# Kernel optimization log

Measured on AMD Instinct MI355X. Metric: run time of the kernel, lower is better.

The kernel has to match this reference:

```python
import jax, jax.numpy as jnp
import numpy as np

DIM = 256
HEADS = 8
DIM_HEAD = 64
EPS = 1e-12  # F.normalize eps


def rms_norm(x, w, dim):
    # F.normalize over channel dim (axis=1) * weight * sqrt(dim)
    n = jnp.sqrt(jnp.sum(x * x, axis=1, keepdims=True))
    xn = x / jnp.maximum(n, EPS)
    return xn * w[None, :, None, None] * (dim ** 0.5)


def setup_inputs() -> dict:
    key = jax.random.key(0)
    ks = jax.random.split(key, 4)
    hd = HEADS * DIM_HEAD
    return {
        "x": jax.random.normal(ks[0], (16, DIM, 64, 64), dtype=jnp.float32),
        "norm_w": jnp.ones((DIM,), jnp.float32),
        "qkv_w": jax.random.normal(ks[1], (3 * hd, DIM), jnp.float32) * (DIM ** -0.5),
        "out_w": jax.random.normal(ks[2], (DIM, hd), jnp.float32) * (hd ** -0.5),
        "out_b": jnp.zeros((DIM,), jnp.float32),
        "out_norm_w": jnp.ones((DIM,), jnp.float32),
    }


def reference(x, norm_w, qkv_w, out_w, out_b, out_norm_w):
    b, c, H, W = x.shape
    n = H * W
    scale = DIM_HEAD ** -0.5

    xn = rms_norm(x, norm_w, DIM)
    # 1x1 conv == channel matmul: [3hd, c] x [b, c, H, W]
    qkv = jnp.einsum('oc,bchw->bohw', qkv_w, xn)
    q, k, v = jnp.split(qkv, 3, axis=1)

    def to_heads(t):
        # b (h d) x y -> b h d n
        return t.reshape(b, HEADS, DIM_HEAD, n)

    q = jax.nn.softmax(to_heads(q), axis=2) * scale  # softmax over feature dim d
    k = jax.nn.softmax(to_heads(k), axis=3)          # softmax over spatial n
    v = to_heads(v)

    ctx = jnp.einsum('bhdn,bhen->bhde', k, v)   # [b,h,d,e]
    out = jnp.einsum('bhde,bhdn->bhen', ctx, q) # [b,h,e,n]
    out = out.reshape(b, HEADS * DIM_HEAD, H, W)

    out = jnp.einsum('oc,bchw->bohw', out_w, out) + out_b[None, :, None, None]
    return rms_norm(out, out_norm_w, DIM)
```

## Files before the change

### kernel.cpp

```cpp
#include <hip/hip_runtime.h>

#define C_ 256
#define N_ 4096
#define NH_ 8

typedef unsigned short u16;
typedef unsigned int u32;
typedef __attribute__((ext_vector_type(8))) short s8v;
typedef __attribute__((ext_vector_type(4))) float f4v;

#define MFMA16 __builtin_amdgcn_mfma_f32_16x16x32_bf16

__device__ __forceinline__ float bf2f(u16 b){ union{u32 u; float f;} v; v.u=((u32)b)<<16; return v.f; }
__device__ __forceinline__ u16 f2bf(float f){ union{float f; u32 u;} v; v.f=f; return (u16)((v.u + 0x7FFFu + ((v.u>>16)&1u))>>16); }

__device__ __forceinline__ void gl_lds16(const u16* g, u16* l){
  __builtin_amdgcn_global_load_lds((const __attribute__((address_space(1))) u32*)g,
                                   (__attribute__((address_space(3))) u32*)l, 16, 0, 0);
}

__global__ __launch_bounds__(256) void k_prep(const float* __restrict__ x, const float* __restrict__ nw,
                                              u16* __restrict__ xnT){
  __shared__ float red[256];
  __shared__ float nws[256];
  const int tid = threadIdx.x;
  nws[tid] = nw[tid];
  const int blk = blockIdx.x, b = blk>>6, n0 = (blk&63)*64;
  const int cq = tid>>6, px = tid&63;
  const float* xp = x + (size_t)b*(C_*N_) + (size_t)(cq*64)*N_ + n0 + px;
  float v[64]; float s = 0.f;
  #pragma unroll
  for (int i=0;i<64;i++){ float t = xp[(size_t)i*N_]; v[i]=t; s = fmaf(t,t,s); }
  red[tid] = s;
  __syncthreads();
  const float st = red[px] + red[64+px] + red[128+px] + red[192+px];
  const float r = 16.0f / fmaxf(sqrtf(st), 1e-12f);
  u16* o = xnT + ((size_t)b*4096 + n0 + px)*256 + cq*64;
  #pragma unroll
  for (int i=0;i<64;i+=2){
    *(u32*)(o+i) = (u32)f2bf(v[i]*r*nws[cq*64+i]) | ((u32)f2bf(v[i+1]*r*nws[cq*64+i+1])<<16);
  }
}

__global__ __launch_bounds__(256) void k_wconv(const float* __restrict__ qkvw, const float* __restrict__ ow,
                                               u16* __restrict__ wqkv, u16* __restrict__ owb){
  int q = blockIdx.x*256 + threadIdx.x;
  int i = q*4;
  const float4 f4 = (i < 393216) ? *(const float4*)&qkvw[i] : *(const float4*)&ow[i-393216];
  u32 lo = (u32)f2bf(f4.x) | ((u32)f2bf(f4.y)<<16);
  u32 hi = (u32)f2bf(f4.z) | ((u32)f2bf(f4.w)<<16);
  u16* dst = (i < 393216) ? (wqkv + i) : (owb + (i-393216));
  *(u32*)dst = lo;
  *(u32*)(dst+2) = hi;
}

__global__ __launch_bounds__(256,3) void k_kv(const u16* __restrict__ xnT, const u16* __restrict__ wqkv,
    u16* __restrict__ ctxp, float* __restrict__ Mp, float* __restrict__ Sp){
  __shared__ u16 xs[64*256];
  __shared__ u16 pbuf[64*72];
  __shared__ u16 vbuf[64*72];
  const int idx = blockIdx.x;
  const int ch = idx&7, h = (idx>>3)&7, b = idx>>6;
  const int tid=threadIdx.x, w=tid>>6, l=tid&63, l15=l&15, lg=l>>4;
  const int swl = (l15&7)<<4;
  const u16* xb  = xnT + (size_t)b*(4096*256);
  const int srow = (l>>5);
  const int scolB = (l&31)*16;
  s8v ak[8], av[8];
  {
    const u16* wkp = wqkv + (size_t)(512 + h*64 + w*16 + l15)*256 + lg*8;
    #pragma unroll
    for (int cs=0; cs<8; cs++){ ak[cs] = *(const s8v*)(wkp + cs*32); av[cs] = *(const s8v*)(wkp + 131072 + cs*32); }
  }
  int colOff[8];
  #pragma unroll
  for (int cs=0; cs<8; cs++) colOff[cs] = (((cs<<6)+(lg<<4)) ^ swl)>>1;

  f4v acc[4];
  #pragma unroll
  for (int et=0;et<4;et++) acc[et] = (f4v){0.f,0.f,0.f,0.f};
  float ps[4] = {0.f,0.f,0.f,0.f};

  {
    const int n0 = ch*512;
    #pragma unroll
    for (int i=0;i<8;i++){
      int rloc = w*16 + i*2 + srow;
      int scol = scolB ^ ((rloc&7)<<4);
      gl_lds16(xb + (size_t)(n0+rloc)*256 + (scol>>1), &xs[(w*16+i*2)*256]);
    }
  }

  for (int t=0; t<8; ++t){
    __syncthreads();
    f4v kacc[4], vacc[4];
    #pragma unroll
    for (int ns=0;ns<4;ns++){ kacc[ns]=(f4v){0.f,0.f,0.f,0.f}; vacc[ns]=(f4v){0.f,0.f,0.f,0.f}; }
    #pragma unroll
    for (int cs=0; cs<8; cs++){
      #pragma unroll
      for (int ns=0; ns<4; ns++){
        s8v bfr = *(const s8v*)&xs[(ns*16+l15)*256 + colOff[cs]];
        kacc[ns] = MFMA16(ak[cs], bfr, kacc[ns], 0,0,0);
        vacc[ns] = MFMA16(av[cs], bfr, vacc[ns], 0,0,0);
      }
    }
    #pragma unroll
    for (int j=0;j<4;j++){
      const int row = w*16 + lg*4 + j;
      #pragma unroll
      for (int ns=0;ns<4;ns++){
        float e = __expf(kacc[ns][j] - 30.0f);
        ps[j] += e;
        pbuf[row*72 + ns*16+l15] = f2bf(e);
        vbuf[row*72 + ns*16+l15] = f2bf(vacc[ns][j]);
      }
    }
    __syncthreads();
    if (t<7){
      const int n0 = ch*512 + (t+1)*64;
      #pragma unroll
      for (int i=0;i<8;i++){
        int rloc = w*16 + i*2 + srow;
        int scol = scolB ^ ((rloc&7)<<4);
        gl_lds16(xb + (size_t)(n0+rloc)*256 + (scol>>1), &xs[(w*16+i*2)*256]);
      }
    }
    #pragma unroll
    for (int ks=0; ks<2; ks++){
      s8v af = *(const s8v*)(pbuf + (w*16+l15)*72 + ks*32 + lg*8);
      #pragma unroll
      for (int et=0; et<4; et++){
        s8v bv = *(const s8v*)(vbuf + (et*16+l15)*72 + ks*32 + lg*8);
        acc[et] = MFMA16(af, bv, acc[et], 0,0,0);
      }
    }
  }
  u16* cp = ctxp + (((size_t)ch*16 + b)*8 + h)*4096;
  #pragma unroll
  for (int et=0; et<4; et++)
    #pragma unroll
    for (int j=0;j<4;j++)
      cp[(w*16+lg*4+j)*64 + et*16+l15] = f2bf(acc[et][j]);
  #pragma unroll
  for (int j=0;j<4;j++){
    float s = ps[j];
    s += __shfl_xor(s,1); s += __shfl_xor(s,2);
    s += __shfl_xor(s,4); s += __shfl_xor(s,8);
    ps[j] = s;
  }
  if (l15==0){
    #pragma unroll
    for (int j=0;j<4;j++){
      int rg = (b*8+h)*64 + w*16 + lg*4 + j;
      Mp[ch*8192+rg]=30.0f; Sp[ch*8192+rg]=ps[j];
    }
  }
}

__global__ __launch_bounds__(256) void k_comb(const u16* __restrict__ ctxp, const float* __restrict__ Mp,
    const float* __restrict__ Sp, u16* __restrict__ ctxD){
  __shared__ float fs[8][64];
  __shared__ float iSs[64];
  const int bh = blockIdx.x, tid = threadIdx.x;
  if (tid < 64){
    float m[8];
    float Mg = -1e30f;
    #pragma unroll
    for (int ch=0;ch<8;ch++){ m[ch] = Mp[ch*8192 + bh*64 + tid]; Mg = fmaxf(Mg, m[ch]); }
    float Sg = 0.f;
    #pragma unroll
    for (int ch=0;ch<8;ch++){
      float fv = __expf(m[ch]-Mg);
      fs[ch][tid] = fv;
      Sg += Sp[ch*8192 + bh*64 + tid]*fv;
    }
    iSs[tid] = 1.0f / Sg;
  }
  __syncthreads();
  const int d = tid>>2, e0 = (tid&3)*16;
  u16* op = ctxD + (size_t)bh*4096 + d*64 + e0;
  const float fsc = iSs[d];
  #pragma unroll
  for (int i=0;i<16;i++){
    float v = 0.f;
    #pragma unroll
    for (int ch=0;ch<8;ch++)
      v += bf2f(ctxp[(size_t)ch*524288 + (size_t)bh*4096 + d*64 + e0+i]) * fs[ch][d];
    op[i] = f2bf(v * fsc);
  }
}

__global__ __launch_bounds__(256) void k_g(const u16* __restrict__ owb, const u16* __restrict__ ctxD,
                                           u16* __restrict__ G){
  const int bh = blockIdx.x, h = bh&7;
  const int tid = threadIdx.x, w = tid>>6, l = tid&63, l15 = l&15, lg = l>>4;
  s8v a[4][2], bD[4][2];
  #pragma unroll
  for (int mt=0; mt<4; mt++)
    #pragma unroll
    for (int ks=0; ks<2; ks++)
      a[mt][ks] = *(const s8v*)(owb + (size_t)(w*64+mt*16+l15)*512 + h*64 + ks*32 + lg*8);
  #pragma unroll
  for (int dt=0; dt<4; dt++)
    #pragma unroll
    for (int ks=0; ks<2; ks++)
      bD[dt][ks] = *(const s8v*)(ctxD + (size_t)bh*4096 + (dt*16+l15)*64 + ks*32 + lg*8);
  f4v acc[4][4];
  #pragma unroll
  for (int mt=0;mt<4;mt++)
    #pragma unroll
    for (int dt=0;dt<4;dt++) acc[mt][dt] = (f4v){0.f,0.f,0.f,0.f};
  #pragma unroll
  for (int ks=0; ks<2; ks++)
    #pragma unroll
    for (int mt=0; mt<4; mt++)
      #pragma unroll
      for (int dt=0; dt<4; dt++)
        acc[mt][dt] = MFMA16(a[mt][ks], bD[dt][ks], acc[mt][dt], 0,0,0);
  u16* gp = G + (size_t)bh*16384;
  #pragma unroll
  for (int mt=0; mt<4; mt++)
    #pragma unroll
    for (int dt=0; dt<4; dt++)
      #pragma unroll
      for (int j=0; j<4; j++)
        gp[(w*64 + mt*16 + lg*4 + j)*64 + dt*16 + l15] = f2bf(acc[mt][dt][j]);
}

__global__ __launch_bounds__(512,4) void k_qout(const u16* __restrict__ xnT, const u16* __restrict__ wqkv,
    const u16* __restrict__ Gg, const float* __restrict__ ob, const float* __restrict__ onw,
    float* __restrict__ out){
  __shared__ u16 WQ[64*256];
  __shared__ u16 Gs[256*64];
  __shared__ u16 qa[4][1024];
  __shared__ float pp[4][2][16];
  __shared__ float ssb[4][2][16];
  const int tid = threadIdx.x;
  const int w=tid>>6, l=tid&63, l15=l&15, lg=l>>4;
  const int g=w&3, half=w>>2;
  const int blk=blockIdx.x, b=blk>>6, n0=(blk&63)*64;
  const u16* xb = xnT + ((size_t)b*4096 + n0)*256;
  const u16* Gbase = Gg + (size_t)b*8*16384;
  u16* qag = qa[g];
  const int wqRow0 = (l>>5);
  const int wqColB = (l&31)*16;
  const int gRow0  = (l>>3);
  const int gColB  = (l&7)*16;
  s8v ax[8];
  #pragma unroll
  for (int cs=0;cs<8;cs++) ax[cs] = *(const s8v*)(xb + (size_t)(g*16+l15)*256 + cs*32 + lg*8);
  f4v oacc[8];
  #pragma unroll
  for (int mt=0;mt<8;mt++) oacc[mt] = (f4v){0.f,0.f,0.f,0.f};

  #pragma unroll
  for (int i=0;i<4;i++){
    int row = (i*8+w)*2 + wqRow0;
    int scol = wqColB ^ ((row&15)<<4);
    gl_lds16(wqkv + (size_t)row*256 + (scol>>1), &WQ[(i*8+w)*512]);
  }
  #pragma unroll
  for (int i=0;i<4;i++){
    int row = (i*8+w)*8 + gRow0;
    int scol = gColB ^ ((row&7)<<4);
    gl_lds16(Gbase + (size_t)row*64 + (scol>>1), &Gs[(i*8+w)*512]);
  }

  for (int h=0; h<8; ++h){
    __syncthreads();
    if (h>0){
      const u16* gg = Gbase + (size_t)h*16384;
      #pragma unroll
      for (int i=0;i<4;i++){
        int row = (i*8+w)*8 + gRow0;
        int scol = gColB ^ ((row&7)<<4);
        gl_lds16(gg + (size_t)row*64 + (scol>>1), &Gs[(i*8+w)*512]);
      }
    }
    f4v qacc[2];
    qacc[0] = (f4v){0.f,0.f,0.f,0.f};
    qacc[1] = (f4v){0.f,0.f,0.f,0.f};
    #pragma unroll
    for (int dt2=0; dt2<2; dt2++){
      const int drow = (half*2+dt2)*16 + l15;
      #pragma unroll
      for (int cs=0; cs<8; cs++){
        s8v bw = *(const s8v*)&WQ[drow*256 + ((((cs<<6)|(lg<<4)) ^ (l15<<4))>>1)];
        qacc[dt2] = MFMA16(ax[cs], bw, qacc[dt2], 0,0,0);
      }
    }
    float sj[4];
    #pragma unroll
    for (int j=0;j<4;j++){
      float e0 = __expf(qacc[0][j]-30.0f);
      float e1 = __expf(qacc[1][j]-30.0f);
      qacc[0][j]=e0; qacc[1][j]=e1;
      float s = e0+e1;
      s += __shfl_xor(s,1); s += __shfl_xor(s,2);
      s += __shfl_xor(s,4); s += __shfl_xor(s,8);
      sj[j] = s;
      if (l15==0) pp[g][half][lg*4+j] = s;
    }
    __syncthreads();
    #pragma unroll
    for (int j=0;j<4;j++){
      const float inv = 0.125f/(sj[j] + pp[g][half^1][lg*4+j]);
      const int row = lg*4+j;
      qag[((row<<6) + (half*2+0)*16 + l15) ^ ((row&7)<<3)] = f2bf(qacc[0][j]*inv);
      qag[((row<<6) + (half*2+1)*16 + l15) ^ ((row&7)<<3)] = f2bf(qacc[1][j]*inv);
    }
    __syncthreads();
    if (h<7){
      const u16* wqg = wqkv + (size_t)(h+1)*64*256;
      #pragma unroll
      for (int i=0;i<4;i++){
        int row = (i*8+w)*2 + wqRow0;
        int scol = wqColB ^ ((row&15)<<4);
        gl_lds16(wqg + (size_t)row*256 + (scol>>1), &WQ[(i*8+w)*512]);
      }
    }
    #pragma unroll
    for (int ks=0; ks<2; ks++){
      s8v ba = *(const s8v*)&qag[(l15<<6) + ((((ks<<6)|(lg<<4)) ^ ((l15&7)<<4))>>1)];
      #pragma unroll
      for (int mt=0; mt<8; mt++){
        s8v aw = *(const s8v*)&Gs[(half*128 + mt*16 + l15)*64 + ((((ks<<6)|(lg<<4)) ^ ((l15&7)<<4))>>1)];
        oacc[mt] = MFMA16(aw, ba, oacc[mt], 0,0,0);
      }
    }
  }
  float ss = 0.f;
  #pragma unroll
  for (int mt=0;mt<8;mt++){
    const float4 o4 = *(const float4*)&ob[half*128 + mt*16 + lg*4];
    #pragma unroll
    for (int j=0;j<4;j++){
      float v = oacc[mt][j] + ((const float*)&o4)[j];
      oacc[mt][j] = v;
      ss = fmaf(v,v,ss);
    }
  }
  ss += __shfl_xor(ss, 16);
  ss += __shfl_xor(ss, 32);
  if (l < 16) ssb[g][half][l15] = ss;
  __syncthreads();
  const float sst = ss + ssb[g][half^1][l15];
  const float r = 16.0f / fmaxf(sqrtf(sst), 1e-12f);
  float* op = out + (size_t)b*(256*4096) + n0 + g*16 + l15;
  #pragma unroll
  for (int mt=0;mt<8;mt++){
    const float4 w4 = *(const float4*)&onw[half*128 + mt*16 + lg*4];
    #pragma unroll
    for (int j=0;j<4;j++){
      int cout = half*128 + mt*16 + lg*4 + j;
      op[(size_t)cout*4096] = oacc[mt][j] * r * ((const float*)&w4)[j];
    }
  }
}

extern "C" void kernel_launch(void* const* d_in, const int* in_sizes, int n_in,
                              void* d_out, int out_size, void* d_ws, size_t ws_size,
                              hipStream_t stream){
  const float* x    = (const float*)d_in[0];
  const float* nw   = (const float*)d_in[1];
  const float* qkvw = (const float*)d_in[2];
  const float* ow   = (const float*)d_in[3];
  const float* ob   = (const float*)d_in[4];
  const float* onw  = (const float*)d_in[5];
  float* out = (float*)d_out;
  char* ws = (char*)d_ws;
  u16*   xnT  = (u16*)(ws);
  u16*   wqkv = (u16*)(ws + 33554432);
  u16*   owb  = (u16*)(ws + 34340864);
  u16*   ctxD = (u16*)(ws + 34603008);
  u16*   ctxp = (u16*)(ws + 35651584);
  u16*   G    = ctxp;
  float* Mp   = (float*)(ws + 44040192);
  float* Sp   = (float*)(ws + 44302336);
  (void)in_sizes; (void)n_in; (void)out_size; (void)ws_size;

  k_wconv<<<512, 256, 0, stream>>>(qkvw, ow, wqkv, owb);
  k_prep <<<1024, 256, 0, stream>>>(x, nw, xnT);
  k_kv   <<<1024, 256, 0, stream>>>(xnT, wqkv, ctxp, Mp, Sp);
  k_comb <<<128, 256, 0, stream>>>(ctxp, Mp, Sp, ctxD);
  k_g    <<<128, 256, 0, stream>>>(owb, ctxD, G);
  k_qout <<<1024, 512, 0, stream>>>(xnT, wqkv, G, ob, onw, out);
}
```

Baseline: 169.4 us.

## Enlarge k_qout tiles to 128 pixels per 1024-thread block

The output kernel now covers 128 pixels per block with 16 waves instead of 64 pixels with 8 waves, halving the grid. Each per-head load of the Q weight slice and the G matrix into shared memory is now reused by twice as many pixels, halving that global-to-LDS traffic. The prefetch of the next head's Q weights is also issued one barrier earlier so it can overlap the softmax normalisation. The cost is a larger shared-memory footprint per block, an aggressive launch bound that may squeeze registers, and a coarser grid.

```diff
diff --git a/kernel.cpp b/kernel.cpp
--- a/kernel.cpp
+++ b/kernel.cpp
@@ -228,43 +228,43 @@
         gp[(w*64 + mt*16 + lg*4 + j)*64 + dt*16 + l15] = f2bf(acc[mt][dt][j]);
 }
 
-__global__ __launch_bounds__(512,4) void k_qout(const u16* __restrict__ xnT, const u16* __restrict__ wqkv,
+__global__ __launch_bounds__(1024,4) void k_qout(const u16* __restrict__ xnT, const u16* __restrict__ wqkv,
     const u16* __restrict__ Gg, const float* __restrict__ ob, const float* __restrict__ onw,
     float* __restrict__ out){
   __shared__ u16 WQ[64*256];
   __shared__ u16 Gs[256*64];
-  __shared__ u16 qa[4][1024];
-  __shared__ float pp[4][2][16];
-  __shared__ float ssb[4][2][16];
+  __shared__ u16 qa[8][1024];
+  __shared__ float pp[8][2][16];
+  __shared__ float ssb[8][2][16];
   const int tid = threadIdx.x;
   const int w=tid>>6, l=tid&63, l15=l&15, lg=l>>4;
-  const int g=w&3, half=w>>2;
-  const int blk=blockIdx.x, b=blk>>6, n0=(blk&63)*64;
+  const int pg=w&7, dh=w>>3;
+  const int blk=blockIdx.x, b=blk>>5, n0=(blk&31)*128;
   const u16* xb = xnT + ((size_t)b*4096 + n0)*256;
   const u16* Gbase = Gg + (size_t)b*8*16384;
-  u16* qag = qa[g];
-  const int wqRow0 = (l>>5);
-  const int wqColB = (l&31)*16;
-  const int gRow0  = (l>>3);
-  const int gColB  = (l&7)*16;
+  u16* qaw = qa[pg];
+  const int wqSrow = l>>5, wqColB = (l&31)*16;
+  const int gSrow  = l>>3, gColB  = (l&7)*16;
   s8v ax[8];
   #pragma unroll
-  for (int cs=0;cs<8;cs++) ax[cs] = *(const s8v*)(xb + (size_t)(g*16+l15)*256 + cs*32 + lg*8);
+  for (int cs=0;cs<8;cs++) ax[cs] = *(const s8v*)(xb + (size_t)(pg*16+l15)*256 + cs*32 + lg*8);
   f4v oacc[8];
   #pragma unroll
   for (int mt=0;mt<8;mt++) oacc[mt] = (f4v){0.f,0.f,0.f,0.f};
 
   #pragma unroll
-  for (int i=0;i<4;i++){
-    int row = (i*8+w)*2 + wqRow0;
+  for (int i=0;i<2;i++){
+    int r2 = (i*16+w)*2;
+    int row = r2 + wqSrow;
     int scol = wqColB ^ ((row&15)<<4);
-    gl_lds16(wqkv + (size_t)row*256 + (scol>>1), &WQ[(i*8+w)*512]);
-  }
-  #pragma unroll
-  for (int i=0;i<4;i++){
-    int row = (i*8+w)*8 + gRow0;
+    gl_lds16(wqkv + (size_t)row*256 + (scol>>1), &WQ[r2*256]);
+  }
+  #pragma unroll
+  for (int i=0;i<2;i++){
+    int r8 = (i*16+w)*8;
+    int row = r8 + gSrow;
     int scol = gColB ^ ((row&7)<<4);
-    gl_lds16(Gbase + (size_t)row*64 + (scol>>1), &Gs[(i*8+w)*512]);
+    gl_lds16(Gbase + (size_t)row*64 + (scol>>1), &Gs[r8*64]);
   }
 
   for (int h=0; h<8; ++h){
@@ -272,10 +272,11 @@
     if (h>0){
       const u16* gg = Gbase + (size_t)h*16384;
       #pragma unroll
-      for (int i=0;i<4;i++){
-        int row = (i*8+w)*8 + gRow0;
+      for (int i=0;i<2;i++){
+        int r8 = (i*16+w)*8;
+        int row = r8 + gSrow;
         int scol = gColB ^ ((row&7)<<4);
-        gl_lds16(gg + (size_t)row*64 + (scol>>1), &Gs[(i*8+w)*512]);
+        gl_lds16(gg + (size_t)row*64 + (scol>>1), &Gs[r8*64]);
       }
     }
     f4v qacc[2];
@@ -283,7 +284,7 @@
     qacc[1] = (f4v){0.f,0.f,0.f,0.f};
     #pragma unroll
     for (int dt2=0; dt2<2; dt2++){
-      const int drow = (half*2+dt2)*16 + l15;
+      const int drow = (dh*2+dt2)*16 + l15;
       #pragma unroll
       for (int cs=0; cs<8; cs++){
         s8v bw = *(const s8v*)&WQ[drow*256 + ((((cs<<6)|(lg<<4)) ^ (l15<<4))>>1)];
@@ -300,32 +301,33 @@
       s += __shfl_xor(s,1); s += __shfl_xor(s,2);
       s += __shfl_xor(s,4); s += __shfl_xor(s,8);
       sj[j] = s;
-      if (l15==0) pp[g][half][lg*4+j] = s;
-    }
-    __syncthreads();
-    #pragma unroll
-    for (int j=0;j<4;j++){
-      const float inv = 0.125f/(sj[j] + pp[g][half^1][lg*4+j]);
+      if (l15==0) pp[pg][dh][lg*4+j] = s;
+    }
+    __syncthreads();
+    if (h<7){
+      const u16* wqg = wqkv + (size_t)(h+1)*16384;
+      #pragma unroll
+      for (int i=0;i<2;i++){
+        int r2 = (i*16+w)*2;
+        int row = r2 + wqSrow;
+        int scol = wqColB ^ ((row&15)<<4);
+        gl_lds16(wqg + (size_t)row*256 + (scol>>1), &WQ[r2*256]);
+      }
+    }
+    #pragma unroll
+    for (int j=0;j<4;j++){
+      const float inv = 0.125f/(sj[j] + pp[pg][dh^1][lg*4+j]);
       const int row = lg*4+j;
-      qag[((row<<6) + (half*2+0)*16 + l15) ^ ((row&7)<<3)] = f2bf(qacc[0][j]*inv);
-      qag[((row<<6) + (half*2+1)*16 + l15) ^ ((row&7)<<3)] = f2bf(qacc[1][j]*inv);
-    }
-    __syncthreads();
-    if (h<7){
-      const u16* wqg = wqkv + (size_t)(h+1)*64*256;
-      #pragma unroll
-      for (int i=0;i<4;i++){
-        int row = (i*8+w)*2 + wqRow0;
-        int scol = wqColB ^ ((row&15)<<4);
-        gl_lds16(wqg + (size_t)row*256 + (scol>>1), &WQ[(i*8+w)*512]);
-      }
-    }
+      qaw[((row<<6) + (dh*2+0)*16 + l15) ^ ((row&7)<<3)] = f2bf(qacc[0][j]*inv);
+      qaw[((row<<6) + (dh*2+1)*16 + l15) ^ ((row&7)<<3)] = f2bf(qacc[1][j]*inv);
+    }
+    __syncthreads();
     #pragma unroll
     for (int ks=0; ks<2; ks++){
-      s8v ba = *(const s8v*)&qag[(l15<<6) + ((((ks<<6)|(lg<<4)) ^ ((l15&7)<<4))>>1)];
+      s8v ba = *(const s8v*)&qaw[(l15<<6) + ((((ks<<6)|(lg<<4)) ^ ((l15&7)<<4))>>1)];
       #pragma unroll
       for (int mt=0; mt<8; mt++){
-        s8v aw = *(const s8v*)&Gs[(half*128 + mt*16 + l15)*64 + ((((ks<<6)|(lg<<4)) ^ ((l15&7)<<4))>>1)];
+        s8v aw = *(const s8v*)&Gs[(dh*128 + mt*16 + l15)*64 + ((((ks<<6)|(lg<<4)) ^ ((l15&7)<<4))>>1)];
         oacc[mt] = MFMA16(aw, ba, oacc[mt], 0,0,0);
       }
     }
@@ -333,7 +335,7 @@
   float ss = 0.f;
   #pragma unroll
   for (int mt=0;mt<8;mt++){
-    const float4 o4 = *(const float4*)&ob[half*128 + mt*16 + lg*4];
+    const float4 o4 = *(const float4*)&ob[dh*128 + mt*16 + lg*4];
     #pragma unroll
     for (int j=0;j<4;j++){
       float v = oacc[mt][j] + ((const float*)&o4)[j];
@@ -343,17 +345,17 @@
   }
   ss += __shfl_xor(ss, 16);
   ss += __shfl_xor(ss, 32);
-  if (l < 16) ssb[g][half][l15] = ss;
+  if (l < 16) ssb[pg][dh][l] = ss;
   __syncthreads();
-  const float sst = ss + ssb[g][half^1][l15];
+  const float sst = ss + ssb[pg][dh^1][l15];
   const float r = 16.0f / fmaxf(sqrtf(sst), 1e-12f);
-  float* op = out + (size_t)b*(256*4096) + n0 + g*16 + l15;
+  float* op = out + (size_t)b*(256*4096) + n0 + pg*16 + l15;
   #pragma unroll
   for (int mt=0;mt<8;mt++){
-    const float4 w4 = *(const float4*)&onw[half*128 + mt*16 + lg*4];
-    #pragma unroll
-    for (int j=0;j<4;j++){
-      int cout = half*128 + mt*16 + lg*4 + j;
+    const float4 w4 = *(const float4*)&onw[dh*128 + mt*16 + lg*4];
+    #pragma unroll
+    for (int j=0;j<4;j++){
+      int cout = dh*128 + mt*16 + lg*4 + j;
       op[(size_t)cout*4096] = oacc[mt][j] * r * ((const float*)&w4)[j];
     }
   }
@@ -385,5 +387,5 @@
   k_kv   <<<1024, 256, 0, stream>>>(xnT, wqkv, ctxp, Mp, Sp);
   k_comb <<<128, 256, 0, stream>>>(ctxp, Mp, Sp, ctxD);
   k_g    <<<128, 256, 0, stream>>>(owb, ctxD, G);
-  k_qout <<<1024, 512, 0, stream>>>(xnT, wqkv, G, ob, onw, out);
-}
+  k_qout <<<512, 1024, 0, stream>>>(xnT, wqkv, G, ob, onw, out);
+}
```

Measured after the change: 164.1 us. 1.03x faster.
